# Optimization experiments

Hardware: AMD Instinct MI355X
Metric: run time of the kernel (lower is better)

The kernel has to match this reference:

```python
import jax, jax.numpy as jnp
import numpy as np

D_MODEL = 1024
NHEAD = 16
HEAD_DIM = D_MODEL // NHEAD


def setup_inputs() -> dict:
    key = jax.random.key(0)
    ks = jax.random.split(key, 9)
    B, T = 2, 2048
    s = 1.0 / np.sqrt(D_MODEL)
    return {
        "sequence": jax.random.normal(ks[0], (B, T, D_MODEL), dtype=jnp.float32),
        "wq": jax.random.normal(ks[1], (D_MODEL, D_MODEL), dtype=jnp.float32) * s,
        "bq": jax.random.normal(ks[2], (D_MODEL,), dtype=jnp.float32) * 0.01,
        "wk": jax.random.normal(ks[3], (D_MODEL, D_MODEL), dtype=jnp.float32) * s,
        "bk": jax.random.normal(ks[4], (D_MODEL,), dtype=jnp.float32) * 0.01,
        "wv": jax.random.normal(ks[5], (D_MODEL, D_MODEL), dtype=jnp.float32) * s,
        "bv": jax.random.normal(ks[6], (D_MODEL,), dtype=jnp.float32) * 0.01,
        "wo": jax.random.normal(ks[7], (D_MODEL, D_MODEL), dtype=jnp.float32) * s,
        "bo": jax.random.normal(ks[8], (D_MODEL,), dtype=jnp.float32) * 0.01,
    }


def reference(sequence, wq, bq, wk, bk, wv, bv, wo, bo):
    B, T, C = sequence.shape
    scale = jnp.asarray(HEAD_DIM ** 0.5, sequence.dtype)
    # projections (nn.Linear: x @ W.T + b)
    def proj(x, w, b):
        y = x @ w.T + b
        return y.reshape(B, T, NHEAD, HEAD_DIM).transpose(0, 2, 1, 3)  # [B,H,T,Dh]
    q = proj(sequence, wq, bq)
    k = proj(sequence, wk, bk)
    v = proj(sequence, wv, bv)
    scores = jnp.einsum("bhqd,bhkd->bhqk", q, k) / scale
    causal = jnp.tril(jnp.ones((T, T), dtype=bool))
    scores = jnp.where(causal, scores, jnp.asarray(-jnp.inf, scores.dtype))
    attn = jax.nn.softmax(scores, axis=-1)
    out = jnp.einsum("bhqk,bhkd->bhqd", attn, v)
    out = out.transpose(0, 2, 1, 3).reshape(B, T, C)
    return out @ wo.T + bo
```

## Files before the change

### kernel.cpp

```cpp
#include <hip/hip_runtime.h>
#include <hip/hip_bf16.h>
#include <hip/hip_fp16.h>
#include <type_traits>

#define DM 1024
#define NH 16
#define HD 64
#define BATCH 2
#define SEQ 2048
#define MROWS (BATCH*SEQ)

typedef __hip_bfloat16 bf16;
typedef __attribute__((ext_vector_type(8))) short    bf16x8;
typedef __attribute__((ext_vector_type(8))) short    s16x8;
typedef __attribute__((ext_vector_type(8))) _Float16 f16x8;
typedef __attribute__((ext_vector_type(4))) _Float16 f16x4;
typedef __attribute__((ext_vector_type(4))) short    s16x4;
typedef __attribute__((ext_vector_type(4))) float    f32x4;

#define LOG2E 1.44269504f
#define M_FIX 4.0f

__device__ __forceinline__ short f2bf(float x) {
    union { float f; unsigned u; } v; v.f = x;
    unsigned r = v.u + 0x7FFF + ((v.u >> 16) & 1);
    return (short)(r >> 16);
}

__device__ __forceinline__ bf16x8 ld8f(const float* p) {
    const float4 a = *(const float4*)p;
    const float4 b = *(const float4*)(p + 4);
    bf16x8 r;
    r[0]=f2bf(a.x); r[1]=f2bf(a.y); r[2]=f2bf(a.z); r[3]=f2bf(a.w);
    r[4]=f2bf(b.x); r[5]=f2bf(b.y); r[6]=f2bf(b.z); r[7]=f2bf(b.w);
    return r;
}

__device__ __forceinline__ void gload_lds16(const void* g, void* l) {
    __builtin_amdgcn_global_load_lds(
        (const __attribute__((address_space(1))) void*)g,
        (__attribute__((address_space(3))) void*)l, 16, 0, 0);
}

__global__ __launch_bounds__(256)
void cvt_bf16(const float* __restrict__ s0, const float* __restrict__ s1,
              const float* __restrict__ s2, const float* __restrict__ s3,
              const float* __restrict__ s4,
              short* d0, short* d1, short* d2, short* d3, short* d4)
{
    const int y = blockIdx.y;
    const float* src = (y==0? s0 : y==1? s1 : y==2? s2 : y==3? s3 : s4);
    short*       dst = (y==0? d0 : y==1? d1 : y==2? d2 : y==3? d3 : d4);
    const int n = (y == 0) ? MROWS*DM : DM*DM;
    const int i = (blockIdx.x * 256 + threadIdx.x) * 8;
    if (i < n) *(bf16x8*)(dst + i) = ld8f(src + i);
}

template<int MODE>
__device__ __forceinline__
void gemm_epilogue(f32x4 (&acc)[4][4], const float* bi, void* out, int z,
                   int tile_m, int tile_n, int wm, int wn,
                   int fr, int quad, int lane, short* lA)
{
    if (MODE == 1 && z == 2) {
        __syncthreads();
        short* sc = lA + (int)(threadIdx.x >> 6) * 256;
        const int rd = lane >> 2, tc = lane & 3;
        #pragma unroll
        for (int mi = 0; mi < 4; ++mi) {
            #pragma unroll
            for (int ni = 0; ni < 4; ++ni) {
                const int colg = tile_n + wn + ni*16 + fr;
                const float bia = bi[colg];
                f16x4 w;
                #pragma unroll
                for (int r = 0; r < 4; ++r) w[r] = (_Float16)(acc[mi][ni][r] + bia);
                *(f16x4*)(sc + fr*16 + quad*4) = w;
                const f16x4 vv = *(const f16x4*)(sc + rd*16 + tc*4);
                const int dg = tile_n + wn + ni*16 + rd;
                const int tg = tile_m + wm + mi*16 + tc*4;
                const int hh = dg >> 6, dd = dg & (HD-1);
                const int bb = tg >> 11, tt = tg & (SEQ-1);
                const int kt = tt >> 5, tko = tt & 31;
                *(f16x4*)((_Float16*)out +
                    ((((size_t)(bb*NH + hh))*(SEQ/32) + kt)*HD + dd)*32 + tko) = vv;
            }
        }
    } else {
        #pragma unroll
        for (int mi = 0; mi < 4; ++mi) {
            #pragma unroll
            for (int ni = 0; ni < 4; ++ni) {
                const int colg = tile_n + wn + ni*16 + fr;
                const float bia = bi[colg];
                #pragma unroll
                for (int r = 0; r < 4; ++r) {
                    const int rowg = tile_m + wm + mi*16 + quad*4 + r;
                    const float v = acc[mi][ni][r] + bia;
                    if (MODE == 0) {
                        ((float*)out)[(size_t)rowg*DM + colg] = v;
                    } else {
                        const int bb = rowg >> 11, t = rowg & (SEQ-1);
                        const int h  = colg >> 6,  d = colg & (HD-1);
                        ((_Float16*)out)[(((size_t)(bb*NH + h))*SEQ + t)*HD + d] = (_Float16)v;
                    }
                }
            }
        }
    }
}

template<int MODE>
__global__ __launch_bounds__(256)
void gemm_a(const short* __restrict__ A,
            const short* __restrict__ W0, const short* __restrict__ W1, const short* __restrict__ W2,
            const float* __restrict__ b0, const float* __restrict__ b1, const float* __restrict__ b2,
            void* o0, void* o1, void* o2)
{
    __shared__ __align__(16) short lA[128*32];
    __shared__ __align__(16) short lB[128*32];

    const int tid  = threadIdx.x;
    const int wid  = tid >> 6;
    const int lane = tid & 63;
    const int tile_n = blockIdx.x * 128;
    const int tile_m = blockIdx.y * 128;
    const int z = blockIdx.z;

    const short* Wg = (z == 0 ? W0 : (z == 1 ? W1 : W2));
    const float* bi = (z == 0 ? b0 : (z == 1 ? b1 : b2));
    void*        out = (z == 0 ? o0 : (z == 1 ? o1 : o2));

    const int sa_row = tile_m + wid*32 + (lane >> 2);
    const int sb_row = tile_n + wid*32 + (lane >> 2);
    const int scol   = (lane & 3) * 8;
    short* lA0 = lA + wid*1024 + lane*8;
    short* lA1 = lA0 + 512;
    short* lB0 = lB + wid*1024 + lane*8;
    short* lB1 = lB0 + 512;

    const int wm = (wid >> 1) * 64;
    const int wn = (wid & 1) * 64;
    const int fr = lane & 15;
    const int quad = lane >> 4;
    const int fq = quad * 8;

    f32x4 acc[4][4] = {};

    for (int k0 = 0; k0 < DM; k0 += 32) {
        __syncthreads();
        gload_lds16(A  + (size_t)sa_row*DM      + k0 + scol, lA0);
        gload_lds16(A  + (size_t)(sa_row+16)*DM + k0 + scol, lA1);
        gload_lds16(Wg + (size_t)sb_row*DM      + k0 + scol, lB0);
        gload_lds16(Wg + (size_t)(sb_row+16)*DM + k0 + scol, lB1);
        __syncthreads();

        bf16x8 af[4], bfv[4];
        #pragma unroll
        for (int i = 0; i < 4; ++i) af[i]  = *(const bf16x8*)(lA + (wm + i*16 + fr)*32 + fq);
        #pragma unroll
        for (int i = 0; i < 4; ++i) bfv[i] = *(const bf16x8*)(lB + (wn + i*16 + fr)*32 + fq);

        #pragma unroll
        for (int mi = 0; mi < 4; ++mi)
            #pragma unroll
            for (int ni = 0; ni < 4; ++ni)
                acc[mi][ni] = __builtin_amdgcn_mfma_f32_16x16x32_bf16(
                    af[mi], bfv[ni], acc[mi][ni], 0, 0, 0);
    }
    gemm_epilogue<MODE>(acc, bi, out, z, tile_m, tile_n, wm, wn, fr, quad, lane, lA);
}

template<typename TA, int MODE>
__global__ __launch_bounds__(256)
void gemm_f(const TA* __restrict__ A,
            const float* __restrict__ W0, const float* __restrict__ W1, const float* __restrict__ W2,
            const float* __restrict__ b0, const float* __restrict__ b1, const float* __restrict__ b2,
            void* o0, void* o1, void* o2)
{
    __shared__ __align__(16) short lA[128*32];
    __shared__ __align__(16) short lB[128*32];

    const int tid  = threadIdx.x;
    const int wid  = tid >> 6;
    const int lane = tid & 63;
    const int tile_n = blockIdx.x * 128;
    const int tile_m = blockIdx.y * 128;
    const int z = blockIdx.z;

    const float* Wg = (z == 0 ? W0 : (z == 1 ? W1 : W2));
    const float* bi = (z == 0 ? b0 : (z == 1 ? b1 : b2));
    void*        out = (z == 0 ? o0 : (z == 1 ? o1 : o2));

    const int sa_row = tile_m + wid*32 + (lane >> 2);
    const int sb_row = tile_n + wid*32 + (lane >> 2);
    const int scol   = (lane & 3) * 8;
    short* lA0 = lA + wid*1024 + lane*8;
    short* lA1 = lA0 + 512;
    short* lB0 = lB + wid*1024 + lane*8;
    short* lB1 = lB0 + 512;

    const int wm = (wid >> 1) * 64;
    const int wn = (wid & 1) * 64;
    const int fr = lane & 15;
    const int quad = lane >> 4;
    const int fq = quad * 8;

    f32x4 acc[4][4] = {};

    for (int k0 = 0; k0 < DM; k0 += 32) {
        bf16x8 ra0, ra1;
        if constexpr (std::is_same<TA, float>::value) {
            ra0 = ld8f((const float*)A + (size_t)sa_row*DM      + k0 + scol);
            ra1 = ld8f((const float*)A + (size_t)(sa_row+16)*DM + k0 + scol);
        } else {
            ra0 = *(const bf16x8*)((const short*)A + (size_t)sa_row*DM      + k0 + scol);
            ra1 = *(const bf16x8*)((const short*)A + (size_t)(sa_row+16)*DM + k0 + scol);
        }
        const bf16x8 rb0 = ld8f(Wg + (size_t)sb_row*DM      + k0 + scol);
        const bf16x8 rb1 = ld8f(Wg + (size_t)(sb_row+16)*DM + k0 + scol);

        __syncthreads();
        *(bf16x8*)lA0 = ra0;
        *(bf16x8*)lA1 = ra1;
        *(bf16x8*)lB0 = rb0;
        *(bf16x8*)lB1 = rb1;
        __syncthreads();

        bf16x8 af[4], bfv[4];
        #pragma unroll
        for (int i = 0; i < 4; ++i) af[i]  = *(const bf16x8*)(lA + (wm + i*16 + fr)*32 + fq);
        #pragma unroll
        for (int i = 0; i < 4; ++i) bfv[i] = *(const bf16x8*)(lB + (wn + i*16 + fr)*32 + fq);

        #pragma unroll
        for (int mi = 0; mi < 4; ++mi)
            #pragma unroll
            for (int ni = 0; ni < 4; ++ni)
                acc[mi][ni] = __builtin_amdgcn_mfma_f32_16x16x32_bf16(
                    af[mi], bfv[ni], acc[mi][ni], 0, 0, 0);
    }
    gemm_epilogue<MODE>(acc, bi, out, z, tile_m, tile_n, wm, wn, fr, quad, lane, lA);
}

__global__ __launch_bounds__(256, 8)
void attn(const _Float16* __restrict__ Q, const _Float16* __restrict__ K,
          const _Float16* __restrict__ Vt, short* __restrict__ O)
{
    __shared__ __align__(16) _Float16 lsK[2][2048];
    __shared__ __align__(16) _Float16 lsV[2][2048];

    const int t    = threadIdx.x;
    const int lane = t & 63;
    const int wid  = t >> 6;
    const int id   = blockIdx.x;
    const int bh   = id & 31;
    const int band = 31 - (id >> 5);
    const size_t base = (size_t)bh * SEQ * HD;
    const int qr = lane & 15;
    const int quad = lane >> 4;
    const int bb = bh >> 4, h = bh & (NH-1);

    const int k_goff = ((t>>2)&31)*64 + (t>>7)*32 + (t&3)*8;
    const int v_goff = (t&63)*32 + (t>>6)*8;

    const float SC1 = 0.125f * LOG2E;
    const float SC2 = -M_FIX * LOG2E;
    const int vboff = (quad>>1)*512 + (quad&1)*4 + qr*8;

    const int q_tile = band*64 + wid*16;
    const int q_idx  = q_tile + qr;
    const int nsubt  = 2*band + 2;
    const int ktm    = 2*band + (wid >> 1);

    const f16x8* Qv = (const f16x8*)(Q + base + (size_t)q_idx*HD);
    const f16x8 qf0 = Qv[quad];
    const f16x8 qf1 = Qv[quad + 4];

    float l_cur = 0.f;
    f32x4 o[4] = {};

    gload_lds16(K  + base + k_goff, &lsK[0][0] + t*8);
    gload_lds16(Vt + base + v_goff, &lsV[0][0] + t*8);

    int cur = 0;
    #pragma unroll 1
    for (int u = 0; u < nsubt; ++u) {
        if (u + 1 < nsubt) {
            const size_t g = base + (size_t)(u + 1)*2048;
            gload_lds16(K  + g + k_goff, &lsK[cur^1][0] + t*8);
            gload_lds16(Vt + g + v_goff, &lsV[cur^1][0] + t*8);
            asm volatile("s_waitcnt vmcnt(2)" ::: "memory");
        } else {
            asm volatile("s_waitcnt vmcnt(0)" ::: "memory");
        }
        __builtin_amdgcn_s_barrier();
        __builtin_amdgcn_sched_barrier(0);

        if (u <= ktm) {
            const _Float16* sK = &lsK[cur][0];
            const _Float16* sV = &lsV[cur][0];

            const f16x8 ka0 = *(const f16x8*)(sK + qr*32 + quad*8);
            const f16x8 ka1 = *(const f16x8*)(sK + 1024 + qr*32 + quad*8);
            const f16x8 kb0 = *(const f16x8*)(sK + (16+qr)*32 + quad*8);
            const f16x8 kb1 = *(const f16x8*)(sK + 1024 + (16+qr)*32 + quad*8);

            __builtin_amdgcn_s_setprio(1);
            f32x4 s0 = {}, s1 = {};
            s0 = __builtin_amdgcn_mfma_f32_16x16x32_f16(ka0, qf0, s0, 0, 0, 0);
            s0 = __builtin_amdgcn_mfma_f32_16x16x32_f16(ka1, qf1, s0, 0, 0, 0);
            s1 = __builtin_amdgcn_mfma_f32_16x16x32_f16(kb0, qf0, s1, 0, 0, 0);
            s1 = __builtin_amdgcn_mfma_f32_16x16x32_f16(kb1, qf1, s1, 0, 0, 0);

            f16x4 p0, p1;
            if (u == ktm) {
                const int k_base = u*32;
                float ls = 0.f;
                #pragma unroll
                for (int r = 0; r < 4; ++r) {
                    const int key = k_base + quad*4 + r;
                    float e0 = exp2f(s0[r] * SC1 + SC2);
                    float e1 = exp2f(s1[r] * SC1 + SC2);
                    e0 = (key      <= q_idx) ? e0 : 0.f;
                    e1 = (key + 16 <= q_idx) ? e1 : 0.f;
                    ls += e0 + e1;
                    p0[r] = (_Float16)e0;
                    p1[r] = (_Float16)e1;
                }
                l_cur += ls;
            } else {
                float ls = 0.f;
                #pragma unroll
                for (int r = 0; r < 4; ++r) {
                    const float e0 = exp2f(s0[r] * SC1 + SC2);
                    const float e1 = exp2f(s1[r] * SC1 + SC2);
                    ls += e0 + e1;
                    p0[r] = (_Float16)e0;
                    p1[r] = (_Float16)e1;
                }
                l_cur += ls;
            }

            #pragma unroll
            for (int dt = 0; dt < 4; ++dt) {
                const f16x4 av0 = *(const f16x4*)(sV + vboff + dt*128);
                const f16x4 av1 = *(const f16x4*)(sV + 1024 + vboff + dt*128);
                o[dt] = __builtin_amdgcn_mfma_f32_16x16x16f16(av0, p0, o[dt], 0, 0, 0);
                o[dt] = __builtin_amdgcn_mfma_f32_16x16x16f16(av1, p1, o[dt], 0, 0, 0);
            }
            __builtin_amdgcn_s_setprio(0);
        }
        __builtin_amdgcn_sched_barrier(0);
        __builtin_amdgcn_s_barrier();
        cur ^= 1;
    }

    l_cur += __shfl_xor(l_cur, 16, 64);
    l_cur += __shfl_xor(l_cur, 32, 64);
    const float linv = 1.0f / fmaxf(l_cur, 1e-30f);

    const int tq = q_tile + qr;
    #pragma unroll
    for (int dt = 0; dt < 4; ++dt) {
        s16x4 pk;
        #pragma unroll
        for (int r = 0; r < 4; ++r) pk[r] = f2bf(o[dt][r] * linv);
        *(s16x4*)(O + ((size_t)(bb*SEQ + tq))*DM + h*HD + dt*16 + quad*4) = pk;
    }
}

extern "C" void kernel_launch(void* const* d_in, const int* in_sizes, int n_in,
                              void* d_out, int out_size, void* d_ws, size_t ws_size,
                              hipStream_t stream)
{
    const float* seq = (const float*)d_in[0];
    const float* wq  = (const float*)d_in[1];
    const float* bq  = (const float*)d_in[2];
    const float* wk  = (const float*)d_in[3];
    const float* bk  = (const float*)d_in[4];
    const float* wv  = (const float*)d_in[5];
    const float* bv  = (const float*)d_in[6];
    const float* wo  = (const float*)d_in[7];
    const float* bo  = (const float*)d_in[8];

    _Float16* Qb = (_Float16*)d_ws;
    _Float16* Kb = Qb + (size_t)MROWS*DM;
    _Float16* Vt = Kb + (size_t)MROWS*DM;
    short*    Ob = (short*)(Vt + (size_t)MROWS*DM);
    short*    sq16 = Ob + (size_t)MROWS*DM;
    short*    wq16 = sq16 + (size_t)MROWS*DM;
    short*    wk16 = wq16 + (size_t)DM*DM;
    short*    wv16 = wk16 + (size_t)DM*DM;
    short*    wo16 = wv16 + (size_t)DM*DM;

    const size_t need = ((size_t)MROWS*DM*2)*5 + ((size_t)DM*DM*2)*4;
    const bool fast = ws_size >= need;

    if (fast) {
        dim3 gc(MROWS*DM/(256*8), 5, 1);
        cvt_bf16<<<gc, 256, 0, stream>>>(seq, wq, wk, wv, wo,
                                         sq16, wq16, wk16, wv16, wo16);

        dim3 g1(DM/128, MROWS/128, 3);
        gemm_a<1><<<g1, 256, 0, stream>>>(sq16, wq16, wk16, wv16, bq, bk, bv,
                                          (void*)Qb, (void*)Kb, (void*)Vt);

        attn<<<dim3(1024), 256, 0, stream>>>(Qb, Kb, Vt, Ob);

        dim3 g3(DM/128, MROWS/128, 1);
        gemm_a<0><<<g3, 256, 0, stream>>>(Ob, wo16, wo16, wo16, bo, bo, bo,
                                          d_out, d_out, d_out);
    } else {
        dim3 g1(DM/128, MROWS/128, 3);
        gemm_f<float, 1><<<g1, 256, 0, stream>>>(seq, wq, wk, wv, bq, bk, bv,
                                                 (void*)Qb, (void*)Kb, (void*)Vt);

        attn<<<dim3(1024), 256, 0, stream>>>(Qb, Kb, Vt, Ob);

        dim3 g3(DM/128, MROWS/128, 1);
        gemm_f<short, 0><<<g3, 256, 0, stream>>>(Ob, wo, wo, wo, bo, bo, bo,
                                                 d_out, d_out, d_out);
    }
}
```

Baseline: 197.8 us.

## Load attention K/V fragments directly from global into registers, dropping LDS staging

The attention kernel no longer stages K and V tiles through double-buffered shared memory with block barriers. Each wave now loads its MFMA fragments straight from global memory into registers, using a two-deep software pipeline (fA/fB) that prefetches the next key tile while computing the current one. Launch bounds drop from 8 to 4 blocks per SM to leave room for the extra registers. This removes the barriers and the LDS round trip. The cost is that the four waves of a block each fetch the same K/V data separately, so it relies on cache hits, uses more registers and runs at lower occupancy.

```diff
diff --git a/kernel.cpp b/kernel.cpp
--- a/kernel.cpp
+++ b/kernel.cpp
@@ -243,13 +243,10 @@
     gemm_epilogue<MODE>(acc, bi, out, z, tile_m, tile_n, wm, wn, fr, quad, lane, lA);
 }
 
-__global__ __launch_bounds__(256, 8)
+__global__ __launch_bounds__(256, 4)
 void attn(const _Float16* __restrict__ Q, const _Float16* __restrict__ K,
           const _Float16* __restrict__ Vt, short* __restrict__ O)
 {
-    __shared__ __align__(16) _Float16 lsK[2][2048];
-    __shared__ __align__(16) _Float16 lsV[2][2048];
-
     const int t    = threadIdx.x;
     const int lane = t & 63;
     const int wid  = t >> 6;
@@ -261,12 +258,8 @@
     const int quad = lane >> 4;
     const int bb = bh >> 4, h = bh & (NH-1);
 
-    const int k_goff = ((t>>2)&31)*64 + (t>>7)*32 + (t&3)*8;
-    const int v_goff = (t&63)*32 + (t>>6)*8;
-
     const float SC1 = 0.125f * LOG2E;
     const float SC2 = -M_FIX * LOG2E;
-    const int vboff = (quad>>1)*512 + (quad&1)*4 + qr*8;
 
     const int q_tile = band*64 + wid*16;
     const int q_idx  = q_tile + qr;
@@ -277,83 +270,86 @@
     const f16x8 qf0 = Qv[quad];
     const f16x8 qf1 = Qv[quad + 4];
 
+    const int koff_a = qr*64 + quad*8;
+    const int koff_b = (16 + qr)*64 + quad*8;
+    const int voff   = qr*32 + (quad>>1)*8 + (quad&1)*4;
+
+    const _Float16* Kb_ = K  + base;
+    const _Float16* Vb_ = Vt + base;
+
     float l_cur = 0.f;
     f32x4 o[4] = {};
 
-    gload_lds16(K  + base + k_goff, &lsK[0][0] + t*8);
-    gload_lds16(Vt + base + v_goff, &lsV[0][0] + t*8);
-
-    int cur = 0;
+    struct Frag { f16x8 ka0, ka1, kb0, kb1; f16x4 av[8]; };
+    Frag fA, fB;
+
+    auto loadF = [&](Frag& f, int kt) {
+        const _Float16* Kp = Kb_ + (size_t)kt*2048;
+        const _Float16* Vp = Vb_ + (size_t)kt*2048;
+        f.ka0 = *(const f16x8*)(Kp + koff_a);
+        f.ka1 = *(const f16x8*)(Kp + koff_a + 32);
+        f.kb0 = *(const f16x8*)(Kp + koff_b);
+        f.kb1 = *(const f16x8*)(Kp + koff_b + 32);
+        #pragma unroll
+        for (int dt = 0; dt < 4; ++dt) {
+            f.av[2*dt]   = *(const f16x4*)(Vp + voff + dt*512);
+            f.av[2*dt+1] = *(const f16x4*)(Vp + voff + dt*512 + 16);
+        }
+    };
+
+    auto compF = [&](const Frag& f, int u) {
+        if (u > ktm) return;
+        __builtin_amdgcn_s_setprio(1);
+        f32x4 s0 = {}, s1 = {};
+        s0 = __builtin_amdgcn_mfma_f32_16x16x32_f16(f.ka0, qf0, s0, 0, 0, 0);
+        s0 = __builtin_amdgcn_mfma_f32_16x16x32_f16(f.ka1, qf1, s0, 0, 0, 0);
+        s1 = __builtin_amdgcn_mfma_f32_16x16x32_f16(f.kb0, qf0, s1, 0, 0, 0);
+        s1 = __builtin_amdgcn_mfma_f32_16x16x32_f16(f.kb1, qf1, s1, 0, 0, 0);
+
+        f16x4 p0, p1;
+        if (u == ktm) {
+            const int k_base = u*32;
+            float ls = 0.f;
+            #pragma unroll
+            for (int r = 0; r < 4; ++r) {
+                const int key = k_base + quad*4 + r;
+                float e0 = exp2f(s0[r] * SC1 + SC2);
+                float e1 = exp2f(s1[r] * SC1 + SC2);
+                e0 = (key      <= q_idx) ? e0 : 0.f;
+                e1 = (key + 16 <= q_idx) ? e1 : 0.f;
+                ls += e0 + e1;
+                p0[r] = (_Float16)e0;
+                p1[r] = (_Float16)e1;
+            }
+            l_cur += ls;
+        } else {
+            float ls = 0.f;
+            #pragma unroll
+            for (int r = 0; r < 4; ++r) {
+                const float e0 = exp2f(s0[r] * SC1 + SC2);
+                const float e1 = exp2f(s1[r] * SC1 + SC2);
+                ls += e0 + e1;
+                p0[r] = (_Float16)e0;
+                p1[r] = (_Float16)e1;
+            }
+            l_cur += ls;
+        }
+
+        #pragma unroll
+        for (int dt = 0; dt < 4; ++dt) {
+            o[dt] = __builtin_amdgcn_mfma_f32_16x16x16f16(f.av[2*dt],   p0, o[dt], 0, 0, 0);
+            o[dt] = __builtin_amdgcn_mfma_f32_16x16x16f16(f.av[2*dt+1], p1, o[dt], 0, 0, 0);
+        }
+        __builtin_amdgcn_s_setprio(0);
+    };
+
+    loadF(fA, 0);
     #pragma unroll 1
-    for (int u = 0; u < nsubt; ++u) {
-        if (u + 1 < nsubt) {
-            const size_t g = base + (size_t)(u + 1)*2048;
-            gload_lds16(K  + g + k_goff, &lsK[cur^1][0] + t*8);
-            gload_lds16(Vt + g + v_goff, &lsV[cur^1][0] + t*8);
-            asm volatile("s_waitcnt vmcnt(2)" ::: "memory");
-        } else {
-            asm volatile("s_waitcnt vmcnt(0)" ::: "memory");
-        }
-        __builtin_amdgcn_s_barrier();
-        __builtin_amdgcn_sched_barrier(0);
-
-        if (u <= ktm) {
-            const _Float16* sK = &lsK[cur][0];
-            const _Float16* sV = &lsV[cur][0];
-
-            const f16x8 ka0 = *(const f16x8*)(sK + qr*32 + quad*8);
-            const f16x8 ka1 = *(const f16x8*)(sK + 1024 + qr*32 + quad*8);
-            const f16x8 kb0 = *(const f16x8*)(sK + (16+qr)*32 + quad*8);
-            const f16x8 kb1 = *(const f16x8*)(sK + 1024 + (16+qr)*32 + quad*8);
-
-            __builtin_amdgcn_s_setprio(1);
-            f32x4 s0 = {}, s1 = {};
-            s0 = __builtin_amdgcn_mfma_f32_16x16x32_f16(ka0, qf0, s0, 0, 0, 0);
-            s0 = __builtin_amdgcn_mfma_f32_16x16x32_f16(ka1, qf1, s0, 0, 0, 0);
-            s1 = __builtin_amdgcn_mfma_f32_16x16x32_f16(kb0, qf0, s1, 0, 0, 0);
-            s1 = __builtin_amdgcn_mfma_f32_16x16x32_f16(kb1, qf1, s1, 0, 0, 0);
-
-            f16x4 p0, p1;
-            if (u == ktm) {
-                const int k_base = u*32;
-                float ls = 0.f;
-                #pragma unroll
-                for (int r = 0; r < 4; ++r) {
-                    const int key = k_base + quad*4 + r;
-                    float e0 = exp2f(s0[r] * SC1 + SC2);
-                    float e1 = exp2f(s1[r] * SC1 + SC2);
-                    e0 = (key      <= q_idx) ? e0 : 0.f;
-                    e1 = (key + 16 <= q_idx) ? e1 : 0.f;
-                    ls += e0 + e1;
-                    p0[r] = (_Float16)e0;
-                    p1[r] = (_Float16)e1;
-                }
-                l_cur += ls;
-            } else {
-                float ls = 0.f;
-                #pragma unroll
-                for (int r = 0; r < 4; ++r) {
-                    const float e0 = exp2f(s0[r] * SC1 + SC2);
-                    const float e1 = exp2f(s1[r] * SC1 + SC2);
-                    ls += e0 + e1;
-                    p0[r] = (_Float16)e0;
-                    p1[r] = (_Float16)e1;
-                }
-                l_cur += ls;
-            }
-
-            #pragma unroll
-            for (int dt = 0; dt < 4; ++dt) {
-                const f16x4 av0 = *(const f16x4*)(sV + vboff + dt*128);
-                const f16x4 av1 = *(const f16x4*)(sV + 1024 + vboff + dt*128);
-                o[dt] = __builtin_amdgcn_mfma_f32_16x16x16f16(av0, p0, o[dt], 0, 0, 0);
-                o[dt] = __builtin_amdgcn_mfma_f32_16x16x16f16(av1, p1, o[dt], 0, 0, 0);
-            }
-            __builtin_amdgcn_s_setprio(0);
-        }
-        __builtin_amdgcn_sched_barrier(0);
-        __builtin_amdgcn_s_barrier();
-        cur ^= 1;
+    for (int u = 0; u < nsubt; u += 2) {
+        loadF(fB, u + 1);
+        compF(fA, u);
+        if (u + 2 < nsubt) loadF(fA, u + 2);
+        compF(fB, u + 1);
     }
 
     l_cur += __shfl_xor(l_cur, 16, 64);
```

New measurement: 289.7 us. 46.4% more time.
